# Kernel tuning notes

Measured on AMD Instinct MI355X. Metric: run time of the kernel, lower is better.

The kernel has to match this reference:

```python
import jax, jax.numpy as jnp
from jax import lax
import numpy as np

STRIDE = 16.0
PRE_NMS_TOPN = 2000
POST_NMS_TOPN = 300
NMS_THRESH = 0.7
BBOX_XFORM_CLIP = float(np.log(1000.0 / 16.0))
NUM_ANCHORS = 15

# ---- Detectron generate_anchors (numpy, done once) ----

def _whctrs(a):
    w = a[2] - a[0] + 1.0
    h = a[3] - a[1] + 1.0
    return w, h, a[0] + 0.5 * (w - 1), a[1] + 0.5 * (h - 1)

def _mkanchors(ws, hs, xc, yc):
    ws = ws[:, None]; hs = hs[:, None]
    return np.hstack([xc - 0.5 * (ws - 1), yc - 0.5 * (hs - 1),
                      xc + 0.5 * (ws - 1), yc + 0.5 * (hs - 1)])

def _ratio_enum(anchor, ratios):
    w, h, xc, yc = _whctrs(anchor)
    size = w * h
    ws = np.round(np.sqrt(size / ratios))
    hs = np.round(ws * ratios)
    return _mkanchors(ws, hs, xc, yc)

def _scale_enum(anchor, scales):
    w, h, xc, yc = _whctrs(anchor)
    return _mkanchors(w * scales, h * scales, xc, yc)

def generate_anchors(stride, sizes, ratios):
    base = np.array([1, 1, stride, stride], dtype=np.float64) - 1
    ra = _ratio_enum(base, np.asarray(ratios, np.float64))
    anchors = np.vstack([_scale_enum(ra[i], np.asarray(sizes, np.float64) / stride)
                         for i in range(ra.shape[0])])
    return anchors.astype(np.float32)

ANCHORS_NP = generate_anchors(STRIDE, (32, 64, 128, 256, 512), (0.5, 1.0, 2.0))

# ---- proposal helpers (jax) ----

def decode_boxes(anchors, deltas):
    w = anchors[:, 2] - anchors[:, 0] + 1.0
    h = anchors[:, 3] - anchors[:, 1] + 1.0
    cx = anchors[:, 0] + 0.5 * w
    cy = anchors[:, 1] + 0.5 * h
    dx, dy = deltas[:, 0], deltas[:, 1]
    dw = jnp.minimum(deltas[:, 2], BBOX_XFORM_CLIP)
    dh = jnp.minimum(deltas[:, 3], BBOX_XFORM_CLIP)
    pcx = dx * w + cx
    pcy = dy * h + cy
    pw = jnp.exp(dw) * w
    ph = jnp.exp(dh) * h
    return jnp.stack([pcx - 0.5 * pw, pcy - 0.5 * ph,
                      pcx + 0.5 * pw - 1.0, pcy + 0.5 * ph - 1.0], axis=-1)

def clip_boxes(b, info):
    hmax = info[0] - 1.0
    wmax = info[1] - 1.0
    return jnp.stack([jnp.clip(b[:, 0], 0.0, wmax), jnp.clip(b[:, 1], 0.0, hmax),
                      jnp.clip(b[:, 2], 0.0, wmax), jnp.clip(b[:, 3], 0.0, hmax)], axis=-1)

def nms_keep(boxes):
    # boxes already sorted by descending score; greedy NMS via scan
    x1, y1, x2, y2 = boxes[:, 0], boxes[:, 1], boxes[:, 2], boxes[:, 3]
    areas = (x2 - x1 + 1.0) * (y2 - y1 + 1.0)
    xx1 = jnp.maximum(x1[:, None], x1[None, :])
    yy1 = jnp.maximum(y1[:, None], y1[None, :])
    xx2 = jnp.minimum(x2[:, None], x2[None, :])
    yy2 = jnp.minimum(y2[:, None], y2[None, :])
    inter = jnp.maximum(xx2 - xx1 + 1.0, 0.0) * jnp.maximum(yy2 - yy1 + 1.0, 0.0)
    iou = inter / (areas[:, None] + areas[None, :] - inter)
    K = boxes.shape[0]

    def body(keep, i):
        sup = jnp.any(keep & (iou[i] > NMS_THRESH))
        keep = keep.at[i].set(~sup)
        return keep, None

    keep, _ = lax.scan(body, jnp.zeros((K,), bool), jnp.arange(K))
    return keep


def setup_inputs() -> dict:
    key = jax.random.key(0)
    ks = jax.random.split(key, 4)
    x = jax.random.normal(ks[0], (2, 1024, 50, 84), jnp.float32)
    conv_w = 0.01 * jax.random.normal(ks[1], (1024, 1024, 3, 3), jnp.float32)
    conv_b = jnp.zeros((1024,), jnp.float32)
    cls_w = 0.01 * jax.random.normal(ks[2], (2 * NUM_ANCHORS, 1024, 1, 1), jnp.float32)
    cls_b = jnp.zeros((2 * NUM_ANCHORS,), jnp.float32)
    bbox_w = 0.01 * jax.random.normal(ks[3], (4 * NUM_ANCHORS, 1024, 1, 1), jnp.float32)
    bbox_b = jnp.zeros((4 * NUM_ANCHORS,), jnp.float32)
    im_info = jnp.array([[800.0, 1344.0, 1.0], [800.0, 1344.0, 1.0]], jnp.float32)
    return {"x": x, "conv_w": conv_w, "conv_b": conv_b, "cls_w": cls_w,
            "cls_b": cls_b, "bbox_w": bbox_w, "bbox_b": bbox_b, "im_info": im_info}


def reference(x, conv_w, conv_b, cls_w, cls_b, bbox_w, bbox_b, im_info):
    A = NUM_ANCHORS
    anchors = jnp.asarray(ANCHORS_NP)
    dn = ('NCHW', 'OIHW', 'NCHW')
    h = jax.nn.relu(lax.conv_general_dilated(x, conv_w, (1, 1), 'SAME',
                                             dimension_numbers=dn) + conv_b[None, :, None, None])
    cls_logits = lax.conv_general_dilated(h, cls_w, (1, 1), 'VALID',
                                          dimension_numbers=dn) + cls_b[None, :, None, None]
    bbox_pred = lax.conv_general_dilated(h, bbox_w, (1, 1), 'VALID',
                                         dimension_numbers=dn) + bbox_b[None, :, None, None]
    B, _, H, W = cls_logits.shape
    # softmax over the 2-way fg/bg axis, take fg prob: [B, A, H, W]
    prob = jax.nn.softmax(cls_logits.reshape(B, 2, A, H, W), axis=1)[:, 1]
    scores = prob.transpose(0, 2, 3, 1).reshape(B, -1)               # [B, H*W*A]
    deltas = bbox_pred.transpose(0, 2, 3, 1).reshape(B, H * W * A, 4)
    # shifted anchor grid, (h, w, a) flatten order matching Detectron
    sy = jnp.arange(H, dtype=jnp.float32) * STRIDE
    sx = jnp.arange(W, dtype=jnp.float32) * STRIDE
    ys, xs = jnp.meshgrid(sy, sx, indexing='ij')
    shifts = jnp.stack([xs, ys, xs, ys], axis=-1).reshape(-1, 4)      # [H*W, 4]
    all_anchors = (shifts[:, None, :] + anchors[None, :, :]).reshape(-1, 4)

    def per_image(sc, dl, info):
        boxes = clip_boxes(decode_boxes(all_anchors, dl), info)
        top_sc, idx = lax.top_k(sc, PRE_NMS_TOPN)
        top_boxes = boxes[idx]
        keep = nms_keep(top_boxes)
        order = jnp.argsort((~keep).astype(jnp.int32))[:POST_NMS_TOPN]  # kept first, score order
        valid = keep[order]
        out_boxes = jnp.where(valid[:, None], top_boxes[order], 0.0)
        out_sc = jnp.where(valid, top_sc[order], 0.0)
        return out_boxes, out_sc

    rois_b, probs_b = jax.vmap(per_image)(scores, deltas, im_info)
    batch_ids = jnp.repeat(jnp.arange(B, dtype=jnp.float32), POST_NMS_TOPN)
    rois = jnp.concatenate([batch_ids[:, None], rois_b.reshape(-1, 4)], axis=1)
    return cls_logits, bbox_pred, rois, probs_b.reshape(-1, 1)
```

## Files before the change

kernel.cpp:

```cpp
#include <hip/hip_runtime.h>
#include <math.h>

#define BATCH   2
#define CIN     1024
#define COUT    1024
#define HH      50
#define WW      84
#define HWX     4200
#define NA      15
#define NSC     63000
#define TOPN    2000
#define POSTN   300
#define CAP     8192
#define CLS_OFF   0
#define BBOX_OFF  252000
#define ROIS_OFF  756000
#define PROBS_OFF 759000

#define TPI 273
#define USTR 274

__constant__ double ANCH[NA][4] = {
  {-15.0,  -4.0,  30.0, 19.0},
  {-38.0, -16.0,  53.0, 31.0},
  {-84.0, -40.0,  99.0, 55.0},
  {-176.0,-88.0, 191.0,103.0},
  {-360.0,-184.0,375.0,199.0},
  {-8.0,  -8.0,  23.0, 23.0},
  {-24.0, -24.0, 39.0, 39.0},
  {-56.0, -56.0, 71.0, 71.0},
  {-120.0,-120.0,135.0,135.0},
  {-248.0,-248.0,263.0,263.0},
  {-3.0, -14.0, 18.0, 29.0},
  {-14.0, -36.0, 29.0, 51.0},
  {-36.0, -80.0, 51.0, 95.0},
  {-80.0,-168.0, 95.0,183.0},
  {-168.0,-344.0,183.0,359.0}
};

__constant__ double BTd[6][6] = {
  {4.0,  0.0, -5.0,  0.0, 1.0, 0.0},
  {0.0, -4.0, -4.0,  1.0, 1.0, 0.0},
  {0.0,  4.0, -4.0, -1.0, 1.0, 0.0},
  {0.0, -2.0, -1.0,  2.0, 1.0, 0.0},
  {0.0,  2.0, -1.0, -2.0, 1.0, 0.0},
  {0.0,  4.0,  0.0, -5.0, 0.0, 1.0}
};
__constant__ double ATd[4][6] = {
  {1.0, 1.0,  1.0, 1.0,  1.0, 0.0},
  {0.0, 1.0, -1.0, 2.0, -2.0, 0.0},
  {0.0, 1.0,  1.0, 4.0,  4.0, 0.0},
  {0.0, 1.0, -1.0, 8.0, -8.0, 1.0}
};

#define BBOX_CLIP 4.1351665567423560

#define WS_WT     0
#define WS_U      98304
#define WS_V      3465216
#define WS_C      16048128
#define WS_H64    19402752
#define OV_H      WS_V
#define OV_SC     (WS_C + 0)
#define OV_TIDX   (WS_C + 126000)
#define OV_TSC    (WS_C + 130000)
#define OV_BOX    (WS_C + 134000)
#define OV_MASK   (WS_C + 166000)

typedef double dx4 __attribute__((ext_vector_type(4)));

__device__ __forceinline__ void gload16(const void* gptr, void* lptr) {
  __builtin_amdgcn_global_load_lds(
      (const __attribute__((address_space(1))) unsigned int*)gptr,
      (__attribute__((address_space(3))) unsigned int*)lptr, 16, 0, 0);
}
#define MFMA64(a, b, c) __builtin_amdgcn_mfma_f64_16x16x4f64(a, b, c, 0, 0, 0)

__launch_bounds__(256)
__global__ void itrans_k(const float* __restrict__ x, double* __restrict__ U,
                         int b, int r) {
  __shared__ float XT[8][6][84];
  const int bx = blockIdx.x;
  const int cg  = bx & 127;
  const int ty  = bx >> 7;
  const int ci0 = cg * 8;
  for (int e = threadIdx.x; e < 4032; e += 256) {
    int ci = e / 504, rem = e % 504;
    int ry = rem / 84, xx = rem % 84;
    int y = ty*4 - 1 + ry;
    float v = 0.f;
    if (y >= 0 && y < HH) v = x[((size_t)(b*CIN + ci0 + ci)*HH + y)*WW + xx];
    XT[ci][ry][xx] = v;
  }
  __syncthreads();
  const int tid = threadIdx.x;
  if (tid < 168) {
    const int ci = tid / 21, tx = tid % 21;
    const double c0 = BTd[r][0], c1 = BTd[r][1], c2 = BTd[r][2];
    const double c3 = BTd[r][3], c4 = BTd[r][4], c5 = BTd[r][5];
    double tt[6];
#pragma unroll
    for (int j = 0; j < 6; ++j) {
      int col = tx*4 - 1 + j;
      double v = 0.0;
      if (col >= 0 && col < WW) {
        v = c0*(double)XT[ci][0][col] + c1*(double)XT[ci][1][col]
          + c2*(double)XT[ci][2][col] + c3*(double)XT[ci][3][col]
          + c4*(double)XT[ci][4][col] + c5*(double)XT[ci][5][col];
      }
      tt[j] = v;
    }
    const int t = ty*21 + tx;
#pragma unroll
    for (int c = 0; c < 6; ++c) {
      double u = BTd[c][0]*tt[0] + BTd[c][1]*tt[1] + BTd[c][2]*tt[2]
               + BTd[c][3]*tt[3] + BTd[c][4]*tt[4] + BTd[c][5]*tt[5];
      U[(size_t)(c*1024 + ci0 + ci)*USTR + t] = u;
    }
  }
}

#define GR0(a,b,c) (0.25*(a))
#define GR1(a,b,c) (-((a)+(b)+(c))*(1.0/6.0))
#define GR2(a,b,c) ((-(a)+(b)-(c))*(1.0/6.0))
#define GR3(a,b,c) (((a)+2.0*(b)+4.0*(c))*(1.0/24.0))
#define GR4(a,b,c) (((a)-2.0*(b)+4.0*(c))*(1.0/24.0))
#define GR5(a,b,c) ((c))
__launch_bounds__(256)
__global__ void wtrans_k(const float* __restrict__ conv_w, double* __restrict__ V,
                         int r) {
  const int g = blockIdx.x*256 + threadIdx.x;
  const int co = g & 1023, ci = g >> 10;
  const float* gp = conv_w + (size_t)(co*1024 + ci)*9;
  double g00 = (double)gp[0], g01 = (double)gp[1], g02 = (double)gp[2];
  double g10 = (double)gp[3], g11 = (double)gp[4], g12 = (double)gp[5];
  double g20 = (double)gp[6], g21 = (double)gp[7], g22 = (double)gp[8];
  double p0, p1, p2;
  switch (r) {
    case 0: p0=GR0(g00,g10,g20); p1=GR0(g01,g11,g21); p2=GR0(g02,g12,g22); break;
    case 1: p0=GR1(g00,g10,g20); p1=GR1(g01,g11,g21); p2=GR1(g02,g12,g22); break;
    case 2: p0=GR2(g00,g10,g20); p1=GR2(g01,g11,g21); p2=GR2(g02,g12,g22); break;
    case 3: p0=GR3(g00,g10,g20); p1=GR3(g01,g11,g21); p2=GR3(g02,g12,g22); break;
    case 4: p0=GR4(g00,g10,g20); p1=GR4(g01,g11,g21); p2=GR4(g02,g12,g22); break;
    default:p0=GR5(g00,g10,g20); p1=GR5(g01,g11,g21); p2=GR5(g02,g12,g22); break;
  }
  const size_t cico = (size_t)ci*1024 + co;
  V[0ull*1048576ull + cico] = GR0(p0,p1,p2);
  V[1ull*1048576ull + cico] = GR1(p0,p1,p2);
  V[2ull*1048576ull + cico] = GR2(p0,p1,p2);
  V[3ull*1048576ull + cico] = GR3(p0,p1,p2);
  V[4ull*1048576ull + cico] = GR4(p0,p1,p2);
  V[5ull*1048576ull + cico] = GR5(p0,p1,p2);
}

__launch_bounds__(256, 2)
__global__ void wgemm_k(const double* __restrict__ U, const double* __restrict__ V,
                        double* __restrict__ C) {
  __shared__ __align__(16) double As[2][32*64];
  __shared__ __align__(16) double Bs[2][32*64];
  const int tid = threadIdx.x;
  const int lane = tid & 63;
  const int w = tid >> 6;
  const int wm = w >> 1, wn = w & 1;
  const int l15 = lane & 15, lq = lane >> 4;
  const int bx = blockIdx.x;
  const int mt = bx >> 4, nt = bx & 15;
  const int t0 = mt * 64, n0 = nt * 64;
  const int z = blockIdx.z;
  const double* Ub = U + (size_t)z * (1024ull*USTR);
  const double* Vb = V + (size_t)z * 1048576ull;
  double* Cb = C + (size_t)z * ((size_t)TPI*1024);

  int pidx[4], nidx[4];
  {
    dx4 pr = {0.,0.,0.,0.}, pc = {0.,0.,0.,0.};
    pr = MFMA64((double)l15, 1.0, pr);
    pc = MFMA64(1.0, (double)l15, pc);
#pragma unroll
    for (int i = 0; i < 4; ++i) {
      pidx[i] = ((int)pr[i]) >> 2;
      nidx[i] = ((int)pc[i]) >> 2;
    }
  }

  auto stage = [&](int k0s, int slot) {
    char* Ad = (char*)&As[slot][0];
    char* Bd = (char*)&Bs[slot][0];
#pragma unroll
    for (int i = 0; i < 4; ++i) {
      int u = tid + i*256;
      int row = u >> 5, cp = u & 31;
      int t = t0 + 2*cp; if (t > 272) t = 272;
      gload16(Ub + (size_t)(k0s + row)*USTR + t, Ad + u*16);
    }
#pragma unroll
    for (int i = 0; i < 4; ++i) {
      int u = tid + i*256;
      int row = u >> 5, cp = u & 31;
      gload16(Vb + (size_t)(k0s + row)*1024 + n0 + 2*cp, Bd + u*16);
    }
  };

  dx4 acc[2][2];
#pragma unroll
  for (int i = 0; i < 2; ++i)
#pragma unroll
    for (int j = 0; j < 2; ++j) acc[i][j] = (dx4){0.,0.,0.,0.};

  stage(0, 0);
  __syncthreads();
  int cur = 0;
#pragma unroll 1
  for (int k0 = 0; k0 < 1024; k0 += 32) {
    if (k0 + 32 < 1024) stage(k0 + 32, cur ^ 1);
    const double* Ap = &As[cur][0];
    const double* Bp = &Bs[cur][0];
#pragma unroll
    for (int kk = 0; kk < 32; kk += 4) {
      const int ar = (kk + lq)*64 + wm*32 + l15;
      double a0 = Ap[ar], a1 = Ap[ar + 16];
      const int br = (kk + lq)*64 + wn*32 + l15;
      double b0 = Bp[br], b1 = Bp[br + 16];
      acc[0][0] = MFMA64(a0, b0, acc[0][0]);
      acc[0][1] = MFMA64(a0, b1, acc[0][1]);
      acc[1][0] = MFMA64(a1, b0, acc[1][0]);
      acc[1][1] = MFMA64(a1, b1, acc[1][1]);
    }
    __syncthreads();
    cur ^= 1;
  }

#pragma unroll
  for (int m2 = 0; m2 < 2; ++m2) {
#pragma unroll
    for (int n2 = 0; n2 < 2; ++n2) {
#pragma unroll
      for (int i = 0; i < 4; ++i) {
        int t = t0 + wm*32 + m2*16 + pidx[i];
        int co = n0 + wn*32 + n2*16 + nidx[i];
        if (t < TPI) Cb[(size_t)t*1024 + co] = acc[m2][n2][i];
      }
    }
  }
}

__launch_bounds__(256)
__global__ void otrans_k(const double* __restrict__ C, double* __restrict__ h64b,
                         int r) {
  const int g = blockIdx.x*256 + threadIdx.x;
  const int co = g & 1023, t = g >> 10;
  double m0 = C[((size_t)0*TPI + t)*1024 + co];
  double m1 = C[((size_t)1*TPI + t)*1024 + co];
  double m2 = C[((size_t)2*TPI + t)*1024 + co];
  double m3 = C[((size_t)3*TPI + t)*1024 + co];
  double m4 = C[((size_t)4*TPI + t)*1024 + co];
  double m5 = C[((size_t)5*TPI + t)*1024 + co];
  double s[4];
#pragma unroll
  for (int bb = 0; bb < 4; ++bb)
    s[bb] = ATd[bb][0]*m0 + ATd[bb][1]*m1 + ATd[bb][2]*m2
          + ATd[bb][3]*m3 + ATd[bb][4]*m4 + ATd[bb][5]*m5;
  const int ty = t / 21, tx = t % 21;
#pragma unroll
  for (int a = 0; a < 4; ++a) {
    const int y = ty*4 + a;
    if (y >= HH) continue;
    const double fa = ATd[a][r];
#pragma unroll
    for (int bb = 0; bb < 4; ++bb) {
      const size_t idx = ((size_t)(y*WW + tx*4 + bb))*1024 + co;
      if (r == 0) h64b[idx] = fa * s[bb];
      else        h64b[idx] += fa * s[bb];
    }
  }
}

__launch_bounds__(256)
__global__ void fin_k(const double* __restrict__ h64, const float* __restrict__ bias,
                      float* __restrict__ h) {
  __shared__ float T[64*65];
  const int m0  = blockIdx.x * 64;
  const int co0 = blockIdx.y * 64;
  const int b   = blockIdx.z;
  const int tid = threadIdx.x;
#pragma unroll
  for (int i = 0; i < 16; ++i) {
    int e = tid + i*256;
    int mi = e >> 6, coi = e & 63;
    int m = m0 + mi;
    double v = 0.0;
    if (m < HWX) v = h64[((size_t)b*HWX + m)*1024 + co0 + coi];
    T[mi*65 + coi] = (float)fmax(v + (double)bias[co0 + coi], 0.0);
  }
  __syncthreads();
#pragma unroll
  for (int i = 0; i < 16; ++i) {
    int e = tid + i*256;
    int coi = e >> 6, mi = e & 63;
    int m = m0 + mi;
    if (m < HWX) h[((size_t)(b*COUT + co0 + coi))*HWX + m] = T[mi*65 + coi];
  }
}

__global__ void wt_k(const float* __restrict__ cls_w, const float* __restrict__ bbox_w,
                     float* __restrict__ wT) {
  int t = blockIdx.x*256 + threadIdx.x;
  if (t >= 96*1024) return;
  int c = t / 96, o = t - (t/96)*96;
  float v = 0.f;
  if (o < 30)      v = cls_w[(size_t)o*1024 + c];
  else if (o < 90) v = bbox_w[(size_t)(o-30)*1024 + c];
  wT[t] = v;
}

__launch_bounds__(256)
__global__ void heads_k(const float* __restrict__ h, const float* __restrict__ wT,
                        const float* __restrict__ cls_b, const float* __restrict__ bbox_b,
                        float* __restrict__ out_cls, float* __restrict__ out_bbox) {
  __shared__ float Hs[32*64];
  __shared__ float Ws[32*96];
  const int tid = threadIdx.x;
  const int b   = blockIdx.y;
  const int m0  = blockIdx.x * 64;
  const int tp  = tid & 15;
  const int to  = tid >> 4;

  double acc[4][6];
  #pragma unroll
  for (int i = 0; i < 4; ++i)
    #pragma unroll
    for (int j = 0; j < 6; ++j) acc[i][j] = 0.0;

  for (int c0 = 0; c0 < CIN; c0 += 32) {
    for (int e = tid; e < 2048; e += 256) {
      int ci = e >> 6, mi = e & 63; int m = m0 + mi;
      Hs[e] = (m < HWX) ? h[((size_t)b*COUT + c0 + ci)*HWX + m] : 0.f;
    }
    for (int e = tid; e < 3072; e += 256) {
      int ci = e / 96, o = e - ci*96;
      Ws[e] = wT[(size_t)(c0 + ci)*96 + o];
    }
    __syncthreads();
    #pragma unroll 8
    for (int ci = 0; ci < 32; ++ci) {
      double a[4], wv[6];
      #pragma unroll
      for (int i = 0; i < 4; ++i) a[i] = (double)Hs[ci*64 + tp*4 + i];
      #pragma unroll
      for (int j = 0; j < 6; ++j) wv[j] = (double)Ws[ci*96 + to*6 + j];
      #pragma unroll
      for (int i = 0; i < 4; ++i)
        #pragma unroll
        for (int j = 0; j < 6; ++j) acc[i][j] += a[i]*wv[j];
    }
    __syncthreads();
  }

  const int mb = m0 + tp*4;
  if (mb < HWX) {
    #pragma unroll
    for (int j = 0; j < 6; ++j) {
      int o = to*6 + j;
      if (o < 30) {
        double bv = (double)cls_b[o];
        float4 v;
        v.x=(float)(acc[0][j]+bv); v.y=(float)(acc[1][j]+bv);
        v.z=(float)(acc[2][j]+bv); v.w=(float)(acc[3][j]+bv);
        *(float4*)&out_cls[((size_t)(b*30 + o))*HWX + mb] = v;
      } else if (o < 90) {
        int ob = o - 30;
        double bv = (double)bbox_b[ob];
        float4 v;
        v.x=(float)(acc[0][j]+bv); v.y=(float)(acc[1][j]+bv);
        v.z=(float)(acc[2][j]+bv); v.w=(float)(acc[3][j]+bv);
        *(float4*)&out_bbox[((size_t)(b*60 + ob))*HWX + mb] = v;
      }
    }
  }
}

__global__ void score_k(const float* __restrict__ out_cls, float* __restrict__ scores) {
  int t = blockIdx.x*256 + threadIdx.x;
  if (t >= BATCH*NSC) return;
  int b = t / NSC; int r = t - b*NSC;
  int m = r / NA;  int a = r - m*NA;
  float l0 = out_cls[((size_t)(b*30 + a))*HWX + m];
  float l1 = out_cls[((size_t)(b*30 + a + NA))*HWX + m];
  double p = 1.0 / (1.0 + exp((double)l0 - (double)l1));
  scores[t] = (float)p;
}

__launch_bounds__(1024)
__global__ void topk_k(const float* __restrict__ scores,
                       unsigned* __restrict__ top_idx, float* __restrict__ top_score) {
  __shared__ unsigned hist[256];
  __shared__ unsigned sh_b1, sh_need, sh_cut, sh_cnt;
  __shared__ unsigned long long key[CAP];
  const int b = blockIdx.x;
  const int tid = threadIdx.x;
  const float* sc = scores + (size_t)b*NSC;

  if (tid < 256) hist[tid] = 0;
  __syncthreads();
  for (int i = tid; i < NSC; i += 1024) {
    unsigned k = __float_as_uint(sc[i]);
    atomicAdd(&hist[k >> 24], 1u);
  }
  __syncthreads();
  if (tid == 0) {
    unsigned cum = 0; int bin = 255;
    for (; bin >= 0; --bin) { cum += hist[bin]; if (cum >= TOPN) break; }
    sh_b1 = (unsigned)bin;
    sh_need = TOPN - (cum - hist[bin]);
  }
  __syncthreads();
  const unsigned b1 = sh_b1, need = sh_need;
  if (tid < 256) hist[tid] = 0;
  __syncthreads();
  for (int i = tid; i < NSC; i += 1024) {
    unsigned k = __float_as_uint(sc[i]);
    if ((k >> 24) == b1) atomicAdd(&hist[(k >> 16) & 255u], 1u);
  }
  __syncthreads();
  if (tid == 0) {
    unsigned cum = 0; int bin = 255;
    for (; bin >= 0; --bin) { cum += hist[bin]; if (cum >= need) break; }
    sh_cut = (b1 << 8) | (unsigned)bin;
    sh_cnt = 0;
  }
  __syncthreads();
  const unsigned cut = sh_cut;
  for (int i = tid; i < CAP; i += 1024) key[i] = 0ull;
  __syncthreads();
  for (int i = tid; i < NSC; i += 1024) {
    unsigned k = __float_as_uint(sc[i]);
    if ((k >> 16) >= cut) {
      unsigned p = atomicAdd(&sh_cnt, 1u);
      if (p < CAP)
        key[p] = ((unsigned long long)k << 32) | (unsigned long long)(0xFFFFFFFFu - (unsigned)i);
    }
  }
  __syncthreads();
  for (int k2 = 2; k2 <= CAP; k2 <<= 1) {
    for (int j = k2 >> 1; j > 0; j >>= 1) {
      for (int i = tid; i < CAP; i += 1024) {
        int p = i ^ j;
        if (p > i) {
          unsigned long long a = key[i], c = key[p];
          bool up = ((i & k2) == 0);
          if (up ? (a < c) : (a > c)) { key[i] = c; key[p] = a; }
        }
      }
      __syncthreads();
    }
  }
  for (int i = tid; i < TOPN; i += 1024) {
    unsigned long long kk = key[i];
    top_idx[(size_t)b*TOPN + i]   = 0xFFFFFFFFu - (unsigned)(kk & 0xFFFFFFFFull);
    top_score[(size_t)b*TOPN + i] = __uint_as_float((unsigned)(kk >> 32));
  }
}

__global__ void decode_k(const unsigned* __restrict__ top_idx,
                         const float* __restrict__ out_bbox,
                         const float* __restrict__ im_info,
                         double* __restrict__ boxesd) {
  int t = blockIdx.x*256 + threadIdx.x;
  if (t >= BATCH*TOPN) return;
  int b = t / TOPN;
  unsigned idx = top_idx[t];
  int a = idx % NA; int m = idx / NA;
  int yy = m / WW;  int xx = m - yy*WW;
  double sx = (double)xx * 16.0, sy = (double)yy * 16.0;
  double A0 = ANCH[a][0] + sx, A1 = ANCH[a][1] + sy;
  double A2 = ANCH[a][2] + sx, A3 = ANCH[a][3] + sy;
  double w_ = A2 - A0 + 1.0, h_ = A3 - A1 + 1.0;
  double cx = A0 + 0.5*w_,  cy = A1 + 0.5*h_;
  const float* bp = out_bbox + (size_t)b*60*HWX;
  double dx = (double)bp[(a*4+0)*HWX + m];
  double dy = (double)bp[(a*4+1)*HWX + m];
  double dw = fmin((double)bp[(a*4+2)*HWX + m], BBOX_CLIP);
  double dh = fmin((double)bp[(a*4+3)*HWX + m], BBOX_CLIP);
  double pcx = dx*w_ + cx, pcy = dy*h_ + cy;
  double pw = exp(dw)*w_,  ph = exp(dh)*h_;
  double x1 = pcx - 0.5*pw, y1 = pcy - 0.5*ph;
  double x2 = pcx + 0.5*pw - 1.0, y2 = pcy + 0.5*ph - 1.0;
  double hmax = (double)im_info[b*3+0] - 1.0;
  double wmax = (double)im_info[b*3+1] - 1.0;
  x1 = fmin(fmax(x1, 0.0), wmax); x2 = fmin(fmax(x2, 0.0), wmax);
  y1 = fmin(fmax(y1, 0.0), hmax); y2 = fmin(fmax(y2, 0.0), hmax);
  boxesd[(size_t)t*4+0] = x1; boxesd[(size_t)t*4+1] = y1;
  boxesd[(size_t)t*4+2] = x2; boxesd[(size_t)t*4+3] = y2;
}

__launch_bounds__(256)
__global__ void iou_k(const double* __restrict__ boxesd,
                      unsigned long long* __restrict__ mask) {
  __shared__ double BX[TOPN*4];
  const int b  = blockIdx.y;
  const int i0 = blockIdx.x * 8;
  const double* src = boxesd + (size_t)b*TOPN*4;
  for (int e = threadIdx.x; e < TOPN*4; e += 256) BX[e] = src[e];
  __syncthreads();
  const int il = threadIdx.x >> 5;
  const int w  = threadIdx.x & 31;
  const int i  = i0 + il;
  double x1 = BX[i*4+0], y1 = BX[i*4+1], x2 = BX[i*4+2], y2 = BX[i*4+3];
  double ai = (x2 - x1 + 1.0)*(y2 - y1 + 1.0);
  unsigned long long bits = 0ull;
  for (int jj = 0; jj < 64; ++jj) {
    int j = w*64 + jj;
    if (j >= TOPN) break;
    double bx1 = BX[j*4+0], by1 = BX[j*4+1], bx2 = BX[j*4+2], by2 = BX[j*4+3];
    double xx1 = fmax(x1, bx1), yy1 = fmax(y1, by1);
    double xx2 = fmin(x2, bx2), yy2 = fmin(y2, by2);
    double iw = fmax(xx2 - xx1 + 1.0, 0.0);
    double ih = fmax(yy2 - yy1 + 1.0, 0.0);
    double inter = iw * ih;
    double aj = (bx2 - bx1 + 1.0)*(by2 - by1 + 1.0);
    double iou = inter / (ai + aj - inter);
    if (iou > 0.7) bits |= (1ull << jj);
  }
  mask[((size_t)b*TOPN + i)*32 + w] = bits;
}

__launch_bounds__(256)
__global__ void nms_out_k(const unsigned long long* __restrict__ mask,
                          const double* __restrict__ boxesd,
                          const float* __restrict__ top_score,
                          float* __restrict__ rois, float* __restrict__ probs) {
  __shared__ unsigned long long MS[256*32];
  __shared__ int kept_idx[POSTN];
  __shared__ int s_cnt, s_done;
  const int b = blockIdx.x;
  const int tid = threadIdx.x;
  if (tid == 0) { s_done = 0; s_cnt = 0; }

  unsigned long long rem = 0ull;
  int cnt = 0;
  const int L = tid;

  for (int ch = 0; ch < 8; ++ch) {
    __syncthreads();
    if (s_done) break;
    const int base = ch * 256;
    for (int e = tid; e < 256*32; e += 256) {
      int row = base + (e >> 5);
      MS[e] = (row < TOPN) ? mask[((size_t)b*TOPN + row)*32 + (e & 31)] : 0ull;
    }
    __syncthreads();
    if (tid < 64) {
      const int lim = (base + 256 < TOPN) ? base + 256 : TOPN;
      int pos = base;
      while (true) {
        unsigned long long wmask = ~rem;
        int lo = pos - 64*L;
        if (lo >= 64) wmask = 0ull;
        else if (lo > 0) wmask &= (~0ull) << lo;
        int hi = lim - 64*L;
        if (hi <= 0) wmask = 0ull;
        else if (hi < 64) wmask &= ((1ull << hi) - 1ull);
        if (L >= 32) wmask = 0ull;
        unsigned long long bal = __ballot(wmask != 0ull);
        if (bal == 0ull) break;
        int lstar = __ffsll((long long)bal) - 1;
        int cand = 64*L + (wmask ? (__ffsll((long long)wmask) - 1) : 0);
        int i = __shfl(cand, lstar);
        if (L == 0) kept_idx[cnt] = i;
        ++cnt;
        if (cnt >= POSTN) {
          if (L == 0) { s_done = 1; }
          break;
        }
        if (L < 32) rem |= MS[(i - base)*32 + L];
        pos = i + 1;
      }
      if (L == 0) s_cnt = cnt;
    }
  }
  __syncthreads();
  const int n = s_cnt;

  for (int j = tid; j < POSTN; j += 256) {
    float* rr = rois + ((size_t)b*POSTN + j)*5;
    rr[0] = (float)b; rr[1] = 0.f; rr[2] = 0.f; rr[3] = 0.f; rr[4] = 0.f;
    probs[(size_t)b*POSTN + j] = 0.f;
  }
  for (int j = tid; j < n; j += 256) {
    int i = kept_idx[j];
    const double* bx = boxesd + ((size_t)b*TOPN + i)*4;
    float* rr = rois + ((size_t)b*POSTN + j)*5;
    rr[1] = (float)bx[0]; rr[2] = (float)bx[1];
    rr[3] = (float)bx[2]; rr[4] = (float)bx[3];
    probs[(size_t)b*POSTN + j] = top_score[(size_t)b*TOPN + i];
  }
}

extern "C" void kernel_launch(void* const* d_in, const int* in_sizes, int n_in,
                              void* d_out, int out_size, void* d_ws, size_t ws_size,
                              hipStream_t stream) {
  const float* x      = (const float*)d_in[0];
  const float* conv_w = (const float*)d_in[1];
  const float* conv_b = (const float*)d_in[2];
  const float* cls_w  = (const float*)d_in[3];
  const float* cls_b  = (const float*)d_in[4];
  const float* bbox_w = (const float*)d_in[5];
  const float* bbox_b = (const float*)d_in[6];
  const float* im_info= (const float*)d_in[7];

  float* out  = (float*)d_out;
  float* out_cls  = out + CLS_OFF;
  float* out_bbox = out + BBOX_OFF;
  float* rois     = out + ROIS_OFF;
  float* probs    = out + PROBS_OFF;

  float* wsf = (float*)d_ws;
  float*    wT      = wsf + WS_WT;
  double*   U       = (double*)(wsf + WS_U);
  double*   V       = (double*)(wsf + WS_V);
  double*   Cws     = (double*)(wsf + WS_C);
  double*   h64     = (double*)(wsf + WS_H64);
  float*    h       = wsf + OV_H;
  float*    scores  = wsf + OV_SC;
  unsigned* top_idx = (unsigned*)(wsf + OV_TIDX);
  float*    top_sc  = wsf + OV_TSC;
  double*   boxesd  = (double*)(wsf + OV_BOX);
  unsigned long long* mask = (unsigned long long*)(wsf + OV_MASK);

  wt_k<<<dim3((96*1024 + 255)/256), dim3(256), 0, stream>>>(cls_w, bbox_w, wT);
  for (int r = 0; r < 6; ++r) {
    wtrans_k<<<dim3(4096), dim3(256), 0, stream>>>(conv_w, V, r);
    for (int b = 0; b < 2; ++b) {
      itrans_k<<<dim3(1664), dim3(256), 0, stream>>>(x, U, b, r);
      wgemm_k<<<dim3(80, 1, 6), dim3(256), 0, stream>>>(U, V, Cws);
      otrans_k<<<dim3(1092), dim3(256), 0, stream>>>(Cws, h64 + (size_t)b*HWX*1024, r);
    }
  }
  fin_k<<<dim3(66, 16, 2), dim3(256), 0, stream>>>(h64, conv_b, h);
  heads_k<<<dim3(66, 2), dim3(256), 0, stream>>>(h, wT, cls_b, bbox_b, out_cls, out_bbox);
  score_k<<<dim3((BATCH*NSC + 255)/256), dim3(256), 0, stream>>>(out_cls, scores);
  topk_k<<<dim3(2), dim3(1024), 0, stream>>>(scores, top_idx, top_sc);
  decode_k<<<dim3((BATCH*TOPN + 255)/256), dim3(256), 0, stream>>>(top_idx, out_bbox, im_info, boxesd);
  iou_k<<<dim3(TOPN/8, 2), dim3(256), 0, stream>>>(boxesd, mask);
  nms_out_k<<<dim3(2), dim3(256), 0, stream>>>(mask, boxesd, top_sc, rois, probs);
}
```

Before: 2.081 ms.

## Rewrite heads GEMM with FP64 MFMA and double-buffered async smem loads

Replaces the scalar FP64 FMA loop in the cls/bbox head GEMM with FP64 MFMA 16x16x4 instructions, using four waves per block that each own a 16x48 output tile. Tile loads now go through 16-byte direct global-to-LDS copies into double-buffered shared memory, so the next K slice is fetched while the current one is computed. The M tile shrinks to 32, which doubles the grid to 132x2 blocks for more parallelism. Each thread's output coordinates are derived by running the MFMA on index values, and the edge tile clamps its load address, which leans on the store-side bounds check to stay correct.

```diff
diff --git a/kernel.cpp b/kernel.cpp
--- a/kernel.cpp
+++ b/kernel.cpp
@@ -313,67 +313,89 @@
   wT[t] = v;
 }
 
-__launch_bounds__(256)
+__launch_bounds__(256, 2)
 __global__ void heads_k(const float* __restrict__ h, const float* __restrict__ wT,
                         const float* __restrict__ cls_b, const float* __restrict__ bbox_b,
                         float* __restrict__ out_cls, float* __restrict__ out_bbox) {
-  __shared__ float Hs[32*64];
-  __shared__ float Ws[32*96];
+  __shared__ __align__(16) float As[2][32*32];
+  __shared__ __align__(16) float Bs[2][32*96];
   const int tid = threadIdx.x;
-  const int b   = blockIdx.y;
-  const int m0  = blockIdx.x * 64;
-  const int tp  = tid & 15;
-  const int to  = tid >> 4;
-
-  double acc[4][6];
-  #pragma unroll
-  for (int i = 0; i < 4; ++i)
-    #pragma unroll
-    for (int j = 0; j < 6; ++j) acc[i][j] = 0.0;
-
+  const int lane = tid & 63;
+  const int w = tid >> 6;
+  const int wm = w >> 1, wn = w & 1;
+  const int l15 = lane & 15, lq = lane >> 4;
+  const int mt = blockIdx.x, b = blockIdx.y;
+  const int m0 = mt * 32;
+
+  int pidx[4], nidx[4];
+  {
+    dx4 pr = {0.,0.,0.,0.}, pc = {0.,0.,0.,0.};
+    pr = MFMA64((double)l15, 1.0, pr);
+    pc = MFMA64(1.0, (double)l15, pc);
+#pragma unroll
+    for (int i = 0; i < 4; ++i) {
+      pidx[i] = ((int)pr[i]) >> 2;
+      nidx[i] = ((int)pc[i]) >> 2;
+    }
+  }
+
+  auto stage = [&](int c0, int slot) {
+    {
+      int row = tid >> 3, cp = tid & 7;
+      int mm = m0 + cp*4; if (mm > HWX - 4) mm = HWX - 4;
+      gload16(h + ((size_t)(b*COUT + c0 + row))*HWX + mm,
+              (char*)&As[slot][0] + tid*16);
+    }
+#pragma unroll
+    for (int i = 0; i < 3; ++i) {
+      int e = tid + i*256;
+      int row = e / 24, q = e % 24;
+      gload16(wT + (size_t)(c0 + row)*96 + q*4,
+              (char*)&Bs[slot][0] + e*16);
+    }
+  };
+
+  dx4 acc[3];
+#pragma unroll
+  for (int j = 0; j < 3; ++j) acc[j] = (dx4){0.,0.,0.,0.};
+
+  stage(0, 0);
+  __syncthreads();
+  int cur = 0;
+#pragma unroll 1
   for (int c0 = 0; c0 < CIN; c0 += 32) {
-    for (int e = tid; e < 2048; e += 256) {
-      int ci = e >> 6, mi = e & 63; int m = m0 + mi;
-      Hs[e] = (m < HWX) ? h[((size_t)b*COUT + c0 + ci)*HWX + m] : 0.f;
-    }
-    for (int e = tid; e < 3072; e += 256) {
-      int ci = e / 96, o = e - ci*96;
-      Ws[e] = wT[(size_t)(c0 + ci)*96 + o];
+    if (c0 + 32 < CIN) stage(c0 + 32, cur ^ 1);
+    const float* Ap = &As[cur][0];
+    const float* Bp = &Bs[cur][0];
+#pragma unroll
+    for (int kk = 0; kk < 32; kk += 4) {
+      double a0 = (double)Ap[(kk + lq)*32 + wm*16 + l15];
+      const int bb = (kk + lq)*96 + wn*48 + l15;
+      double b0 = (double)Bp[bb];
+      double b1 = (double)Bp[bb + 16];
+      double b2 = (double)Bp[bb + 32];
+      acc[0] = MFMA64(a0, b0, acc[0]);
+      acc[1] = MFMA64(a0, b1, acc[1]);
+      acc[2] = MFMA64(a0, b2, acc[2]);
     }
     __syncthreads();
-    #pragma unroll 8
-    for (int ci = 0; ci < 32; ++ci) {
-      double a[4], wv[6];
-      #pragma unroll
-      for (int i = 0; i < 4; ++i) a[i] = (double)Hs[ci*64 + tp*4 + i];
-      #pragma unroll
-      for (int j = 0; j < 6; ++j) wv[j] = (double)Ws[ci*96 + to*6 + j];
-      #pragma unroll
-      for (int i = 0; i < 4; ++i)
-        #pragma unroll
-        for (int j = 0; j < 6; ++j) acc[i][j] += a[i]*wv[j];
-    }
-    __syncthreads();
-  }
-
-  const int mb = m0 + tp*4;
-  if (mb < HWX) {
-    #pragma unroll
-    for (int j = 0; j < 6; ++j) {
-      int o = to*6 + j;
-      if (o < 30) {
-        double bv = (double)cls_b[o];
-        float4 v;
-        v.x=(float)(acc[0][j]+bv); v.y=(float)(acc[1][j]+bv);
-        v.z=(float)(acc[2][j]+bv); v.w=(float)(acc[3][j]+bv);
-        *(float4*)&out_cls[((size_t)(b*30 + o))*HWX + mb] = v;
-      } else if (o < 90) {
-        int ob = o - 30;
-        double bv = (double)bbox_b[ob];
-        float4 v;
-        v.x=(float)(acc[0][j]+bv); v.y=(float)(acc[1][j]+bv);
-        v.z=(float)(acc[2][j]+bv); v.w=(float)(acc[3][j]+bv);
-        *(float4*)&out_bbox[((size_t)(b*60 + ob))*HWX + mb] = v;
+    cur ^= 1;
+  }
+
+#pragma unroll
+  for (int nf = 0; nf < 3; ++nf) {
+#pragma unroll
+    for (int i = 0; i < 4; ++i) {
+      int m = m0 + wm*16 + pidx[i];
+      int o = wn*48 + nf*16 + nidx[i];
+      if (m < HWX) {
+        if (o < 30) {
+          out_cls[((size_t)(b*30 + o))*HWX + m] =
+              (float)(acc[nf][i] + (double)cls_b[o]);
+        } else if (o < 90) {
+          out_bbox[((size_t)(b*60 + (o - 30)))*HWX + m] =
+              (float)(acc[nf][i] + (double)bbox_b[o - 30]);
+        }
       }
     }
   }
@@ -637,7 +659,7 @@
     }
   }
   fin_k<<<dim3(66, 16, 2), dim3(256), 0, stream>>>(h64, conv_b, h);
-  heads_k<<<dim3(66, 2), dim3(256), 0, stream>>>(h, wT, cls_b, bbox_b, out_cls, out_bbox);
+  heads_k<<<dim3(132, 2), dim3(256), 0, stream>>>(h, wT, cls_b, bbox_b, out_cls, out_bbox);
   score_k<<<dim3((BATCH*NSC + 255)/256), dim3(256), 0, stream>>>(out_cls, scores);
   topk_k<<<dim3(2), dim3(1024), 0, stream>>>(scores, top_idx, top_sc);
   decode_k<<<dim3((BATCH*TOPN + 255)/256), dim3(256), 0, stream>>>(top_idx, out_bbox, im_info, boxesd);
```

Result: faster. 1.898 ms (-8.8%).
